# Kernel optimization log

Measured on AMD Instinct MI355X. Metric: run time of the kernel, lower is better.

Reference implementation:

```python
import jax, jax.numpy as jnp
import numpy as np

N = 8192
F_IN = 64
F_OUT = 64
ALPHA = 0.2  # LeakyReLU negative slope
NEG_INF = -9e15


def setup_inputs() -> dict:
    key = jax.random.key(0)
    k1, k2, k3, k4 = jax.random.split(key, 4)
    h = jax.random.normal(k1, (N, F_IN), dtype=jnp.float32)
    adj = jax.random.randint(k2, (N, N), 0, 2, dtype=jnp.int32)
    W = jax.random.normal(k3, (F_OUT, F_IN), dtype=jnp.float32) * (1.0 / np.sqrt(F_IN))
    a = jax.random.normal(k4, (2 * F_OUT,), dtype=jnp.float32) * (1.0 / np.sqrt(2 * F_OUT))
    return {"h": h, "adj": adj, "W": W, "a": a}


def reference(h, adj, W, a):
    # Wh = h @ W.T  (nn.Linear with no bias)
    Wh = h @ W.T  # [N, F_out]
    # The original builds [N*N, 2F] pairs then applies `a`; this is exactly
    # e_ij = leakyrelu(a1 . Wh_i + a2 . Wh_j) -- decomposed form, same math.
    a1, a2 = a[:F_OUT], a[F_OUT:]
    src = Wh @ a1  # [N]
    dst = Wh @ a2  # [N]
    e = jax.nn.leaky_relu(src[:, None] + dst[None, :], negative_slope=ALPHA)  # [N, N]
    scores = jnp.where(adj > 0, e, NEG_INF)
    attention = jax.nn.softmax(scores, axis=1)
    # dropout is identity in eval mode (dropout=0.0)
    h_prime = attention @ Wh  # [N, F_out]
    return jax.nn.elu(h_prime)
```

## Files before the change

### kernel.cpp

```cpp
#include <hip/hip_runtime.h>
#include <hip/hip_bf16.h>

#define NN 8192
#define F 64
#define ALPHA 0.2f
#define L2E 1.44269504f
#define DBOUND 16.0f
#define G 8
#define COLS (NN / G)
#define NSTEPS (COLS / 32)

typedef __attribute__((ext_vector_type(8))) short short8;
typedef __attribute__((ext_vector_type(4))) float f32x4;
typedef __attribute__((ext_vector_type(4))) int i32x4;

__device__ __forceinline__ unsigned fb(float x) {
    return __builtin_bit_cast(unsigned, x);
}
__device__ __forceinline__ short f2bf(float x) {
    union { float f; unsigned u; } v; v.f = x;
    unsigned r = v.u + 0x7FFF + ((v.u >> 16) & 1);
    return (short)(r >> 16);
}

__global__ __launch_bounds__(256) void k_prep(const float* __restrict__ h,
        const float* __restrict__ W, const float* __restrict__ a,
        short* __restrict__ WhTt, float* __restrict__ src, float* __restrict__ dst2) {
    __shared__ float Wl[F][F + 1];
    __shared__ short shT[F][4];
    int tid = threadIdx.x;
    for (int m = 0; m < 4; ++m) {
        int idx = m * 1024 + tid * 4;
        float4 v = *(const float4*)&W[idx];
        int row = idx >> 6, col = idx & 63;
        Wl[row][col] = v.x; Wl[row][col + 1] = v.y;
        Wl[row][col + 2] = v.z; Wl[row][col + 3] = v.w;
    }
    __syncthreads();
    int w = tid >> 6, lane = tid & 63;
    int i = blockIdx.x * 4 + w;
    const float* hrow = &h[(size_t)i * F];
    float wh = 0.f;
    #pragma unroll
    for (int k = 0; k < F; k += 4) {
        float4 hv = *(const float4*)&hrow[k];
        wh += hv.x * Wl[lane][k] + hv.y * Wl[lane][k + 1]
            + hv.z * Wl[lane][k + 2] + hv.w * Wl[lane][k + 3];
    }
    shT[lane][w] = f2bf(wh);
    float s1 = wh * a[lane];
    float s2 = wh * a[F + lane];
    #pragma unroll
    for (int off = 32; off; off >>= 1) {
        s1 += __shfl_xor(s1, off);
        s2 += __shfl_xor(s2, off);
    }
    if (lane == 0) { src[i] = s1; dst2[i] = s2 * L2E; }
    __syncthreads();
    if (tid < F) {
        int f = tid;
        int b = blockIdx.x;
        int t = b >> 3;
        int off = (b * 4) & 31;
        size_t addr = (((size_t)(t * 4 + (f >> 4)) * 64
                       + (off >> 3) * 16 + (f & 15)) << 3) + (off & 7);
        short4 v = make_short4(shT[f][0], shT[f][1], shT[f][2], shT[f][3]);
        *(short4*)&WhTt[addr] = v;
    }
}

__global__ __launch_bounds__(256) void k_mask(const int* __restrict__ adj,
                                              unsigned long long* __restrict__ mg) {
    int w = threadIdx.x >> 6, l = threadIdx.x & 63;
    int gw = blockIdx.x * 4 + w;
    const int NW = 2048 * 4;
    const int NCH = (NN * NN) / 256;
    int sh = 4 * (l & 15);
    #pragma unroll 4
    for (int c = gw; c < NCH; c += NW) {
        size_t base = (size_t)c * 256;
        i32x4 a = __builtin_nontemporal_load((const i32x4*)(adj + base) + l);
        unsigned n = (a.x > 0 ? 1u : 0u) | (a.y > 0 ? 2u : 0u)
                   | (a.z > 0 ? 4u : 0u) | (a.w > 0 ? 8u : 0u);
        unsigned long long v = (unsigned long long)n << sh;
        v |= __shfl_xor(v, 1);
        v |= __shfl_xor(v, 2);
        v |= __shfl_xor(v, 4);
        v |= __shfl_xor(v, 8);
        if ((l & 15) == 0)
            mg[base / 64 + (l >> 4)] = v;
    }
}

__global__ __launch_bounds__(256, 4) void k_attn(const unsigned* __restrict__ maskg,
        const short8* __restrict__ WhTt, const float* __restrict__ src,
        const float* __restrict__ dst2,
        float* __restrict__ Opart, float* __restrict__ lpart) {
    __shared__ unsigned mlds[64][33];
    __shared__ float dlds[COLS];

    int rb = blockIdx.x / G;
    int g  = blockIdx.x % G;
    int jbase = g * COLS;
    int tid = threadIdx.x;

    for (int idx = tid; idx < 64 * (COLS / 32); idx += 256) {
        int rr = idx >> 5, cc = idx & 31;
        mlds[rr][cc] = maskg[(size_t)(rb * 64 + rr) * (NN / 32) + (jbase >> 5) + cc];
    }
    for (int idx = tid; idx < COLS; idx += 256)
        dlds[idx] = dst2[jbase + idx];
    __syncthreads();

    int w = tid >> 6, lane = tid & 63;
    int r = lane & 15, q = lane >> 4;
    int qs = q * 8;
    int i = rb * 64 + w * 16 + r;

    float srcv = src[i];
    float sM = srcv + DBOUND;
    float Mi = fmaxf(sM, ALPHA * sM);
    float sL  = srcv * L2E;
    float MiL = Mi * L2E;
    float C1 = sL - MiL;
    float C2 = fmaf(sL, ALPHA, -MiL);

    f32x4 acc0{}, acc1{}, acc2{}, acc3{}, acc4{};
    short8 ones;
    #pragma unroll
    for (int k = 0; k < 8; ++k) ones[k] = (short)0x3F80;

    const unsigned* mrow = &mlds[w * 16 + r][0];

#define LDB(tt, B0, B1, B2, B3) { \
    const short8* bp = WhTt + (size_t)(g * 32 + (tt)) * 256; \
    B0 = bp[lane]; B1 = bp[64 + lane]; B2 = bp[128 + lane]; B3 = bp[192 + lane]; }

#define PEL(dv, bit, eo) { \
    float t1 = (dv) + C1; \
    float t2 = fmaf((dv), ALPHA, C2); \
    float e = __builtin_amdgcn_exp2f(fmaxf(t1, t2)); \
    eo = (bit) ? e : 0.0f; }

    short8 cb0, cb1, cb2, cb3, nb0, nb1, nb2, nb3;
    LDB(0, cb0, cb1, cb2, cb3)

    #pragma unroll 4
    for (int t = 0; t < NSTEPS; ++t) {
        int tn = (t + 1 < NSTEPS) ? t + 1 : t;
        LDB(tn, nb0, nb1, nb2, nb3)

        unsigned m8 = (mrow[t] >> qs) & 0xffu;
        float4 d0 = *(const float4*)&dlds[t * 32 + qs];
        float4 d1 = *(const float4*)&dlds[t * 32 + qs + 4];

        float e0, e1, e2, e3, e4, e5, e6, e7;
        PEL(d0.x, (m8 & 1u),   e0) PEL(d0.y, (m8 & 2u),   e1)
        PEL(d0.z, (m8 & 4u),   e2) PEL(d0.w, (m8 & 8u),   e3)
        PEL(d1.x, (m8 & 16u),  e4) PEL(d1.y, (m8 & 32u),  e5)
        PEL(d1.z, (m8 & 64u),  e6) PEL(d1.w, (m8 & 128u), e7)

        unsigned w0 = __builtin_amdgcn_perm(fb(e1), fb(e0), 0x07060302u);
        unsigned w1 = __builtin_amdgcn_perm(fb(e3), fb(e2), 0x07060302u);
        unsigned w2 = __builtin_amdgcn_perm(fb(e5), fb(e4), 0x07060302u);
        unsigned w3 = __builtin_amdgcn_perm(fb(e7), fb(e6), 0x07060302u);
        short8 af = __builtin_bit_cast(short8, make_uint4(w0, w1, w2, w3));

        acc0 = __builtin_amdgcn_mfma_f32_16x16x32_bf16(af, cb0, acc0, 0, 0, 0);
        acc1 = __builtin_amdgcn_mfma_f32_16x16x32_bf16(af, cb1, acc1, 0, 0, 0);
        acc2 = __builtin_amdgcn_mfma_f32_16x16x32_bf16(af, cb2, acc2, 0, 0, 0);
        acc3 = __builtin_amdgcn_mfma_f32_16x16x32_bf16(af, cb3, acc3, 0, 0, 0);
        acc4 = __builtin_amdgcn_mfma_f32_16x16x32_bf16(af, ones, acc4, 0, 0, 0);

        cb0 = nb0; cb1 = nb1; cb2 = nb2; cb3 = nb3;
    }
#undef PEL
#undef LDB

    int ic = rb * 64 + w * 16 + q * 4;
    if (r == 0) {
        #pragma unroll
        for (int reg = 0; reg < 4; ++reg)
            lpart[(size_t)g * NN + ic + reg] = acc4[reg];
    }

    size_t ob = (size_t)g * (size_t)(NN * F);
    #pragma unroll
    for (int reg = 0; reg < 4; ++reg) {
        size_t ro = ob + (size_t)(ic + reg) * F + r;
        Opart[ro]      = acc0[reg];
        Opart[ro + 16] = acc1[reg];
        Opart[ro + 32] = acc2[reg];
        Opart[ro + 48] = acc3[reg];
    }
}

__global__ __launch_bounds__(256) void k_reduce(const float* __restrict__ Opart,
        const float* __restrict__ lpart, float* __restrict__ out) {
    int idx = blockIdx.x * 256 + threadIdx.x;
    int i = idx >> 6;
    float o = 0.f, l = 0.f;
    #pragma unroll
    for (int g = 0; g < G; ++g) {
        o += Opart[(size_t)g * (NN * F) + idx];
        l += lpart[(size_t)g * NN + i];
    }
    float hp = o / l;
    out[idx] = hp > 0.f ? hp : __expf(hp) - 1.f;
}

extern "C" void kernel_launch(void* const* d_in, const int* in_sizes, int n_in,
                              void* d_out, int out_size, void* d_ws, size_t ws_size,
                              hipStream_t stream) {
    const float* h  = (const float*)d_in[0];
    const int* adj  = (const int*)d_in[1];
    const float* W  = (const float*)d_in[2];
    const float* a  = (const float*)d_in[3];
    float* out = (float*)d_out;

    char* ws = (char*)d_ws;
    const size_t OFF_WHTT = 0;
    const size_t OFF_SRC  = (1u << 20);
    const size_t OFF_DST  = OFF_SRC + (32u << 10);
    const size_t OFF_LP   = OFF_DST + (32u << 10);
    const size_t OFF_MASK = OFF_LP + (size_t)G * NN * 4;
    const size_t OFF_OP   = OFF_MASK + (size_t)NN * (NN / 8);

    short* WhTt  = (short*)(ws + OFF_WHTT);
    float* src   = (float*)(ws + OFF_SRC);
    float* dst2  = (float*)(ws + OFF_DST);
    float* lpart = (float*)(ws + OFF_LP);
    unsigned long long* maskg = (unsigned long long*)(ws + OFF_MASK);
    float* Opart = (float*)(ws + OFF_OP);

    k_mask<<<2048, 256, 0, stream>>>(adj, maskg);
    k_prep<<<NN / 4, 256, 0, stream>>>(h, W, a, WhTt, src, dst2);
    k_attn<<<(NN / 64) * G, 256, 0, stream>>>((const unsigned*)maskg,
                                              (const short8*)WhTt, src, dst2,
                                              Opart, lpart);
    k_reduce<<<(NN * F) / 256, 256, 0, stream>>>(Opart, lpart, out);
}
```

Measured before the change: 90.25 us.

## Merge mask/prep kernels and fuse split-K reduction into attention via last-block counter

The adjacency bit-packing and the Wh projection now run in one launch, with block ranges assigned to each role, so the two independent stages overlap and one launch disappears. The separate reduce kernel is removed. The last of the G column-group blocks for each row block, found with an atomic counter and threadfences, sums the partial outputs, normalises them and applies ELU. This adds a memset launch and a serial tail done by one block per row block, in exchange for dropping a launch and the Opart traffic of a separate kernel.

Measured after the change: 305.4 us. +238.4%, slower.

```diff
diff --git a/kernel.cpp b/kernel.cpp
--- a/kernel.cpp
+++ b/kernel.cpp
@@ -9,6 +9,7 @@
 #define G 8
 #define COLS (NN / G)
 #define NSTEPS (COLS / 32)
+#define NMASKB 2048
 
 typedef __attribute__((ext_vector_type(8))) short short8;
 typedef __attribute__((ext_vector_type(4))) float f32x4;
@@ -23,12 +24,39 @@
     return (short)(r >> 16);
 }
 
-__global__ __launch_bounds__(256) void k_prep(const float* __restrict__ h,
+__global__ __launch_bounds__(256) void k_mp(const float* __restrict__ h,
         const float* __restrict__ W, const float* __restrict__ a,
-        short* __restrict__ WhTt, float* __restrict__ src, float* __restrict__ dst2) {
+        const int* __restrict__ adj,
+        short* __restrict__ WhTt, float* __restrict__ src,
+        float* __restrict__ dst2, unsigned long long* __restrict__ mg) {
     __shared__ float Wl[F][F + 1];
     __shared__ short shT[F][4];
     int tid = threadIdx.x;
+
+    if (blockIdx.x < NMASKB) {
+        int w = tid >> 6, l = tid & 63;
+        int gw = blockIdx.x * 4 + w;
+        const int NW = NMASKB * 4;
+        const int NCH = (NN * NN) / 256;
+        int sh = 4 * (l & 15);
+        #pragma unroll 4
+        for (int c = gw; c < NCH; c += NW) {
+            size_t base = (size_t)c * 256;
+            i32x4 av = __builtin_nontemporal_load((const i32x4*)(adj + base) + l);
+            unsigned n = (av.x > 0 ? 1u : 0u) | (av.y > 0 ? 2u : 0u)
+                       | (av.z > 0 ? 4u : 0u) | (av.w > 0 ? 8u : 0u);
+            unsigned long long v = (unsigned long long)n << sh;
+            v |= __shfl_xor(v, 1);
+            v |= __shfl_xor(v, 2);
+            v |= __shfl_xor(v, 4);
+            v |= __shfl_xor(v, 8);
+            if ((l & 15) == 0)
+                mg[base / 64 + (l >> 4)] = v;
+        }
+        return;
+    }
+
+    int b = blockIdx.x - NMASKB;
     for (int m = 0; m < 4; ++m) {
         int idx = m * 1024 + tid * 4;
         float4 v = *(const float4*)&W[idx];
@@ -38,7 +66,7 @@
     }
     __syncthreads();
     int w = tid >> 6, lane = tid & 63;
-    int i = blockIdx.x * 4 + w;
+    int i = b * 4 + w;
     const float* hrow = &h[(size_t)i * F];
     float wh = 0.f;
     #pragma unroll
@@ -59,7 +87,6 @@
     __syncthreads();
     if (tid < F) {
         int f = tid;
-        int b = blockIdx.x;
         int t = b >> 3;
         int off = (b * 4) & 31;
         size_t addr = (((size_t)(t * 4 + (f >> 4)) * 64
@@ -69,35 +96,15 @@
     }
 }
 
-__global__ __launch_bounds__(256) void k_mask(const int* __restrict__ adj,
-                                              unsigned long long* __restrict__ mg) {
-    int w = threadIdx.x >> 6, l = threadIdx.x & 63;
-    int gw = blockIdx.x * 4 + w;
-    const int NW = 2048 * 4;
-    const int NCH = (NN * NN) / 256;
-    int sh = 4 * (l & 15);
-    #pragma unroll 4
-    for (int c = gw; c < NCH; c += NW) {
-        size_t base = (size_t)c * 256;
-        i32x4 a = __builtin_nontemporal_load((const i32x4*)(adj + base) + l);
-        unsigned n = (a.x > 0 ? 1u : 0u) | (a.y > 0 ? 2u : 0u)
-                   | (a.z > 0 ? 4u : 0u) | (a.w > 0 ? 8u : 0u);
-        unsigned long long v = (unsigned long long)n << sh;
-        v |= __shfl_xor(v, 1);
-        v |= __shfl_xor(v, 2);
-        v |= __shfl_xor(v, 4);
-        v |= __shfl_xor(v, 8);
-        if ((l & 15) == 0)
-            mg[base / 64 + (l >> 4)] = v;
-    }
-}
-
 __global__ __launch_bounds__(256, 4) void k_attn(const unsigned* __restrict__ maskg,
         const short8* __restrict__ WhTt, const float* __restrict__ src,
         const float* __restrict__ dst2,
-        float* __restrict__ Opart, float* __restrict__ lpart) {
+        float* __restrict__ Opart, float* __restrict__ lpart,
+        int* __restrict__ ctr, float* __restrict__ out) {
     __shared__ unsigned mlds[64][33];
     __shared__ float dlds[COLS];
+    __shared__ int islast;
+    __shared__ float linv[64];
 
     int rb = blockIdx.x / G;
     int g  = blockIdx.x % G;
@@ -193,20 +200,32 @@
         Opart[ro + 32] = acc2[reg];
         Opart[ro + 48] = acc3[reg];
     }
-}
-
-__global__ __launch_bounds__(256) void k_reduce(const float* __restrict__ Opart,
-        const float* __restrict__ lpart, float* __restrict__ out) {
-    int idx = blockIdx.x * 256 + threadIdx.x;
-    int i = idx >> 6;
-    float o = 0.f, l = 0.f;
-    #pragma unroll
-    for (int g = 0; g < G; ++g) {
-        o += Opart[(size_t)g * (NN * F) + idx];
-        l += lpart[(size_t)g * NN + i];
-    }
-    float hp = o / l;
-    out[idx] = hp > 0.f ? hp : __expf(hp) - 1.f;
+
+    __threadfence();
+    __syncthreads();
+    if (tid == 0) islast = (atomicAdd(&ctr[rb], 1) == G - 1);
+    __syncthreads();
+    if (!islast) return;
+    __threadfence();
+
+    if (tid < 64) {
+        float l = 0.f;
+        #pragma unroll
+        for (int gg = 0; gg < G; ++gg)
+            l += lpart[(size_t)gg * NN + rb * 64 + tid];
+        linv[tid] = 1.0f / l;
+    }
+    __syncthreads();
+    for (int k2 = tid; k2 < 64 * F; k2 += 256) {
+        int row = k2 >> 6, col = k2 & 63;
+        size_t base2 = (size_t)(rb * 64 + row) * F + col;
+        float o = 0.f;
+        #pragma unroll
+        for (int gg = 0; gg < G; ++gg)
+            o += Opart[(size_t)gg * (size_t)(NN * F) + base2];
+        float hp = o * linv[row];
+        out[base2] = hp > 0.f ? hp : __expf(hp) - 1.f;
+    }
 }
 
 extern "C" void kernel_launch(void* const* d_in, const int* in_sizes, int n_in,
@@ -224,19 +243,20 @@
     const size_t OFF_DST  = OFF_SRC + (32u << 10);
     const size_t OFF_LP   = OFF_DST + (32u << 10);
     const size_t OFF_MASK = OFF_LP + (size_t)G * NN * 4;
-    const size_t OFF_OP   = OFF_MASK + (size_t)NN * (NN / 8);
+    const size_t OFF_CTR  = OFF_MASK + (size_t)NN * (NN / 8);
+    const size_t OFF_OP   = OFF_CTR + 4096;
 
     short* WhTt  = (short*)(ws + OFF_WHTT);
     float* src   = (float*)(ws + OFF_SRC);
     float* dst2  = (float*)(ws + OFF_DST);
     float* lpart = (float*)(ws + OFF_LP);
     unsigned long long* maskg = (unsigned long long*)(ws + OFF_MASK);
+    int*   ctr   = (int*)(ws + OFF_CTR);
     float* Opart = (float*)(ws + OFF_OP);
 
-    k_mask<<<2048, 256, 0, stream>>>(adj, maskg);
-    k_prep<<<NN / 4, 256, 0, stream>>>(h, W, a, WhTt, src, dst2);
+    hipMemsetAsync(ctr, 0, (NN / 64) * sizeof(int), stream);
+    k_mp<<<NMASKB + NN / 4, 256, 0, stream>>>(h, W, a, adj, WhTt, src, dst2, maskg);
     k_attn<<<(NN / 64) * G, 256, 0, stream>>>((const unsigned*)maskg,
                                               (const short8*)WhTt, src, dst2,
-                                              Opart, lpart);
-    k_reduce<<<(NN * F) / 256, 256, 0, stream>>>(Opart, lpart, out);
-}
+                                              Opart, lpart, ctr, out);
+}
```
